# Kernel tuning notes

Hardware: AMD Instinct MI355X
Metric: run time of the kernel (lower is better)

## Reference

```python
import math
import jax, jax.numpy as jnp
import numpy as np

N_NODES = 100000
N_EDGES = 1200000
N_BASIS = 20
HIDDEN = 50
SILU_NORM = 1.679  # e3nn normalize2mom constant for silu
LMAX_SH = 5
MID_LS = (0, 1, 2, 3, 4)          # middle = 1x0e+1x1o+1x2e+1x3o+1x4e (dim 25)
OUT_L = 2                          # out = 1x2e (dim 5)
TP2_PATHS = ((0, 2), (1, 1), (1, 3), (2, 0), (2, 2), (2, 4), (3, 1), (3, 3), (3, 5), (4, 2), (4, 4))
NUM_NEIGHBORS = 6


def _fact(n):
    return math.factorial(n)


def _cg(j1, m1, j2, m2, j3, m3):
    # Racah formula for Clebsch-Gordan coefficients (complex SH, Condon-Shortley).
    if m1 + m2 != m3:
        return 0.0
    pref = math.sqrt((2 * j3 + 1) * _fact(j1 + j2 - j3) * _fact(j1 - j2 + j3) * _fact(-j1 + j2 + j3) / _fact(j1 + j2 + j3 + 1))
    pref *= math.sqrt(_fact(j1 + m1) * _fact(j1 - m1) * _fact(j2 + m2) * _fact(j2 - m2) * _fact(j3 + m3) * _fact(j3 - m3))
    s = 0.0
    for k in range(j1 + j2 - j3 + 1):
        d = (k, j1 + j2 - j3 - k, j1 - m1 - k, j2 + m2 - k, j3 - j2 + m1 + k, j3 - j1 - m2 + k)
        if min(d) < 0:
            continue
        den = 1.0
        for q in d:
            den *= _fact(q)
        s += (-1.0) ** k / den
    return pref * s


def _u_real(l):
    # change of basis complex SH -> real SH, rows indexed by real m=-l..l
    U = np.zeros((2 * l + 1, 2 * l + 1), dtype=np.complex128)
    U[l, l] = 1.0
    rt2 = math.sqrt(2.0)
    for m in range(1, l + 1):
        U[l + m, l + m] = (-1.0) ** m / rt2
        U[l + m, l - m] = 1.0 / rt2
        U[l - m, l + m] = -1j * (-1.0) ** m / rt2
        U[l - m, l - m] = 1j / rt2
    return U


def _w3j_real(j1, j2, j3):
    # real-basis Wigner 3j tensor (real for even j1+j2+j3, which holds for all paths here)
    Wc = np.zeros((2 * j1 + 1, 2 * j2 + 1, 2 * j3 + 1), dtype=np.complex128)
    for m1 in range(-j1, j1 + 1):
        for m2 in range(-j2, j2 + 1):
            m3 = -(m1 + m2)
            if abs(m3) <= j3:
                Wc[j1 + m1, j2 + m2, j3 + m3] = (-1.0) ** (j1 - j2 - m3) / math.sqrt(2 * j3 + 1) * _cg(j1, m1, j2, m2, j3, -m3)
    U1, U2, U3 = _u_real(j1).conj(), _u_real(j2).conj(), _u_real(j3).conj()
    Wr = np.einsum('abc,ia,jb,kc->ijk', Wc, U1, U2, U3)
    return np.ascontiguousarray(Wr.real.astype(np.float32))


W3J_TP1 = {l: _w3j_real(0, l, l) for l in MID_LS}
W3J_TP2 = {p: _w3j_real(p[0], p[1], OUT_L) for p in TP2_PATHS}


def spherical_harmonics(vec):
    # vec [E,3] -> component-normalized real SH for l=0..5, concatenated [E,36]
    r = jnp.sqrt(jnp.sum(vec * vec, axis=1))
    x, y, z = vec[:, 0] / r, vec[:, 1] / r, vec[:, 2] / r
    phi = jnp.arctan2(y, x)
    s = jnp.sqrt(jnp.clip(1.0 - z * z, 0.0, 1.0))
    # associated Legendre P[l][m] without Condon-Shortley phase
    P = [[None] * (l + 1) for l in range(LMAX_SH + 1)]
    P[0][0] = jnp.ones_like(z)
    for m in range(1, LMAX_SH + 1):
        P[m][m] = (2 * m - 1) * s * P[m - 1][m - 1]
    for m in range(0, LMAX_SH):
        P[m + 1][m] = (2 * m + 1) * z * P[m][m]
    for l in range(2, LMAX_SH + 1):
        for m in range(0, l - 1):
            P[l][m] = ((2 * l - 1) * z * P[l - 1][m] - (l - 1 + m) * P[l - 2][m]) / (l - m)
    blocks = []
    for l in range(LMAX_SH + 1):
        comps = []
        for m in range(-l, l + 1):
            am = abs(m)
            c = math.sqrt((2 * l + 1) * _fact(l - am) / _fact(l + am)) * (math.sqrt(2.0) if m != 0 else 1.0)
            if m < 0:
                ang = jnp.sin(am * phi)
            elif m > 0:
                ang = jnp.cos(am * phi)
            else:
                ang = jnp.ones_like(phi)
            comps.append(c * P[l][am] * ang)
        blocks.append(jnp.stack(comps, axis=1))
    return jnp.concatenate(blocks, axis=1)


def soft_one_hot(d):
    # e3nn soft_one_hot_linspace(basis='smooth_finite', cutoff=True), start=0, end=3
    values = jnp.linspace(0.0, 3.0, N_BASIS + 2)
    step = values[1] - values[0]
    values = values[1:-1]
    diff = (d[:, None] - values[None, :]) / step

    def sus(t):
        safe = jnp.where(t > 0, t, 1.0)
        return jnp.where(t > 0, jnp.exp(-1.0 / safe), 0.0)

    return 1.14136 * math.exp(2.0) * sus(diff + 1.0) * sus(1.0 - diff)


def tp1(x_scalar, sh, w):
    # FullyConnectedTensorProduct(1x0e, sh, middle) with external per-edge weights w [E,5]
    outs = []
    for i, l in enumerate(MID_LS):
        W = W3J_TP1[l][0]                       # [2l+1, 2l+1]
        alpha = math.sqrt(2 * l + 1)            # sqrt(dim_out / fan_in), fan_in = 1
        shl = sh[:, l * l:(l + 1) * (l + 1)]
        outs.append(alpha * w[:, i:i + 1] * x_scalar * (shl @ W))
    return jnp.concatenate(outs, axis=1)        # [E, 25]


def tp2(feat, sh, w):
    # FullyConnectedTensorProduct(middle, sh, 1x2e) with internal weights w [11]
    alpha = math.sqrt((2 * OUT_L + 1) / len(TP2_PATHS))
    out = jnp.zeros((feat.shape[0], 2 * OUT_L + 1), dtype=feat.dtype)
    for p, (l1, l2) in enumerate(TP2_PATHS):
        W = W3J_TP2[(l1, l2)]                   # [2l1+1, 2l2+1, 5]
        f = feat[:, l1 * l1:(l1 + 1) * (l1 + 1)]
        s = sh[:, l2 * l2:(l2 + 1) * (l2 + 1)]
        tmp = jnp.einsum('ei,ijk->ejk', f, W)
        out = out + (alpha * w[p]) * jnp.einsum('ejk,ej->ek', tmp, s)
    return out                                   # [E, 5]


def _forward(x, pos, edge_index, mlp_w1, mlp_w2, tp2_w):
    N = pos.shape[0]
    edge_from = edge_index[:, 0]
    edge_to = edge_index[:, 1]
    Co = jnp.argmax(jnp.bincount(edge_to, length=N))          # torch.mode(edge_to)
    edge_vec = pos[edge_to] - pos[edge_from]
    sh = spherical_harmonics(edge_vec)                         # [E, 36]
    dist = jnp.linalg.norm(edge_vec, axis=1)
    emb = soft_one_hot(dist)                                   # [E, 20]
    h = jax.nn.silu(emb @ mlp_w1 / math.sqrt(N_BASIS)) * SILU_NORM
    tp_w = h @ mlp_w2 / math.sqrt(HIDDEN)                      # [E, 5]
    feat = tp1(x[edge_to], sh, tp_w)                           # [E, 25]
    node = jax.ops.segment_sum(feat, edge_from, num_segments=N) / math.sqrt(float(NUM_NEIGHBORS))
    feat2 = tp2(node[edge_to], sh, tp2_w)                      # [E, 5]
    node2 = jax.ops.segment_sum(feat2, edge_from, num_segments=N)
    return node2[Co]                                           # [5]


def setup_inputs():
    N, E = N_NODES, N_EDGES
    key = jax.random.key(0)
    k = jax.random.split(key, 7)
    pos = 1.5 * jax.random.normal(k[0], (N, 3), dtype=jnp.float32)
    x = jax.random.normal(k[1], (N, 1), dtype=jnp.float32)
    ef = jax.random.randint(k[2], (E,), 0, N, dtype=jnp.int32)
    off = jax.random.randint(k[3], (E,), 1, N, dtype=jnp.int32)
    et = (ef + off) % N                                        # no self loops -> nonzero edge_vec
    edge_index = jnp.stack([ef, et], axis=1)
    mlp_w1 = jax.random.normal(k[4], (N_BASIS, HIDDEN), dtype=jnp.float32)
    mlp_w2 = jax.random.normal(k[5], (HIDDEN, len(MID_LS)), dtype=jnp.float32)
    tp2_w = jax.random.normal(k[6], (len(TP2_PATHS),), dtype=jnp.float32)
    return {'x': x, 'pos': pos, 'edge_index': edge_index, 'mlp_w1': mlp_w1, 'mlp_w2': mlp_w2, 'tp2_w': tp2_w}


def reference(x, pos, edge_index, mlp_w1, mlp_w2, tp2_w):
    return _forward(x, pos, edge_index, mlp_w1, mlp_w2, tp2_w)
```

## Files before the change

kernel.cpp:

```cpp
#include <hip/hip_runtime.h>
#include <math.h>

#define CAP   2048
#define NW3J  (2080*8)


struct WSPtrs {
  unsigned* counts;
  int* flag;
  unsigned long long* key;
  int* co_count;
  int* s_count;
  int* co_edges;
  float* node_acc;
  float* w3j1;
  float* w3j2;
  size_t zero_bytes;
};

__host__ __device__ inline WSPtrs make_ws(char* ws, int N, int Nw, int use_xcc){
  WSPtrs p;
  size_t o = 0;
  p.counts   = (unsigned*)(ws + o);
  o += use_xcc ? (size_t)8 * Nw * 4 : (size_t)N * 4;
  p.flag     = (int*)(ws + o); o += (size_t)N * 4;
  o = (o + 7) & ~(size_t)7;
  p.key      = (unsigned long long*)(ws + o); o += 8;
  p.co_count = (int*)(ws + o); o += 4;
  p.s_count  = (int*)(ws + o); o += 4;
  p.co_edges = (int*)(ws + o); o += (size_t)CAP * 4;
  p.node_acc = (float*)(ws + o); o += (size_t)CAP * 25 * 4;
  p.w3j1     = (float*)(ws + o); o += 165 * 4;
  p.w3j2     = (float*)(ws + o); o += 1915 * 4;
  p.zero_bytes = o;
  return p;
}


__device__ double cg_coef_lut(int j1,int m1,int j2,int m2,int j3,int m3, const double* __restrict__ fact){
  if (m1 + m2 != m3) return 0.0;
  double pref = sqrt((2.0*j3+1.0) * fact[j1+j2-j3] * fact[j1-j2+j3] * fact[-j1+j2+j3]
                     / fact[j1+j2+j3+1]);
  pref *= sqrt(fact[j1+m1]*fact[j1-m1]*fact[j2+m2]*fact[j2-m2]*fact[j3+m3]*fact[j3-m3]);
  double s = 0.0;
  for (int k = 0; k <= j1+j2-j3; ++k){
    int d2 = j1-m1-k, d3 = j2+m2-k, d4 = j3-j2+m1+k, d5 = j3-j1-m2+k;
    if (d2 < 0 || d3 < 0 || d4 < 0 || d5 < 0) continue;
    double den = fact[k]*fact[j1+j2-j3-k]*fact[d2]*fact[d3]*fact[d4]*fact[d5];
    s += ((k & 1) ? -1.0 : 1.0) / den;
  }
  return pref * s;
}

__device__ double wigner_c_val_lut(int j1,int j2,int j3,int m1,int m2,int m3, const double* __restrict__ fact){
  if (m1+m2+m3 != 0) return 0.0;
  int e = j1 - j2 - m3;
  double sign = (e & 1) ? -1.0 : 1.0;
  return sign / sqrt(2.0*j3+1.0) * cg_coef_lut(j1,m1,j2,m2,j3,-m3,fact);
}

__device__ int conjU_row(int l, int i, int* cols, double* re, double* im){
  int mr = i - l;
  const double irt2 = 0.70710678118654752440;
  if (mr == 0){ cols[0]=l; re[0]=1.0; im[0]=0.0; return 1; }
  int m = mr > 0 ? mr : -mr;
  double sgn = (m & 1) ? -1.0 : 1.0;
  if (mr > 0){
    cols[0]=l+m; re[0]=sgn*irt2; im[0]=0.0;
    cols[1]=l-m; re[1]=irt2;     im[1]=0.0;
  } else {
    cols[0]=l+m; re[0]=0.0; im[0]= sgn*irt2;
    cols[1]=l-m; re[1]=0.0; im[1]=-irt2;
  }
  return 2;
}

__device__ void wigner_term(int gid, float* __restrict__ w3j1, float* __restrict__ w3j2,
                            const double* __restrict__ sfact){
  int entry = gid >> 3;
  int combo = gid & 7;
  if (entry >= 165 + 1915) return;
  int j1, j2, j3, ii, jj, kk;
  float* dst;
  if (entry < 165){
    const int l1off[5] = {0,1,10,35,84};
    int l = 4;
    for (int q = 1; q < 5; ++q) if (entry < l1off[q]){ l = q-1; break; }
    int t = entry - l1off[l];
    int n = 2*l+1;
    j1 = 0; j2 = l; j3 = l;
    ii = 0; jj = t / n; kk = t % n;
    dst = &w3j1[entry];
  } else {
    int t2 = entry - 165;
    const int pl1[11]  = {0,1,1,2,2,2,3,3,3,4,4};
    const int pl2[11]  = {2,1,3,0,2,4,1,3,5,2,4};
    const int poff[11] = {0,25,70,175,200,325,550,655,900,1285,1510};
    int p = 10;
    for (int q = 1; q < 11; ++q) if (t2 < poff[q]){ p = q-1; break; }
    int t = t2 - poff[p];
    j1 = pl1[p]; j2 = pl2[p]; j3 = 2;
    int n2q = 2*j2+1;
    ii = t / (n2q*5); int rem = t % (n2q*5); jj = rem / 5; kk = rem % 5;
    dst = &w3j2[t2];
  }
  int c1[2], c2[2], c3[2];
  double r1[2], i1[2], r2[2], i2[2], r3[2], i3[2];
  int n1 = conjU_row(j1, ii, c1, r1, i1);
  int n2 = conjU_row(j2, jj, c2, r2, i2);
  int n3 = conjU_row(j3, kk, c3, r3, i3);
  int a = (combo >> 2) & 1, b = (combo >> 1) & 1, c = combo & 1;
  if (a >= n1 || b >= n2 || c >= n3) return;
  int m1 = c1[a]-j1, m2 = c2[b]-j2, m3 = c3[c]-j3;
  if (m1 + m2 + m3 != 0) return;
  double wc = wigner_c_val_lut(j1,j2,j3,m1,m2,m3,sfact);
  if (wc == 0.0) return;
  double pr = r1[a]*r2[b] - i1[a]*i2[b];
  double pi = r1[a]*i2[b] + i1[a]*r2[b];
  double qr = pr*r3[c] - pi*i3[c];
  atomicAdd(dst, (float)(wc*qr));
}


__device__ void compute_sh36f(float ex, float ey, float ez, float* __restrict__ sh){
  float r = sqrtf(ex*ex + ey*ey + ez*ez);
  float x = ex/r, y = ey/r, z = ez/r;
  float t = 1.0f - z*z;
  t = t < 0.0f ? 0.0f : (t > 1.0f ? 1.0f : t);
  float s = sqrtf(t);
  float rxy = sqrtf(x*x + y*y);
  float c1, s1;
  if (rxy > 1e-30f){ c1 = x/rxy; s1 = y/rxy; } else { c1 = 1.0f; s1 = 0.0f; }
  float cm[6], sm[6];
  cm[0] = 1.0f; sm[0] = 0.0f;
  for (int m = 1; m <= 5; ++m){
    cm[m] = cm[m-1]*c1 - sm[m-1]*s1;
    sm[m] = sm[m-1]*c1 + cm[m-1]*s1;
  }
  float P[6][6];
  P[0][0] = 1.0f;
  for (int m=1;m<=5;m++) P[m][m] = (float)(2*m-1)*s*P[m-1][m-1];
  for (int m=0;m<5;m++)  P[m+1][m] = (float)(2*m+1)*z*P[m][m];
  for (int l=2;l<=5;l++)
    for (int m=0;m<=l-2;m++)
      P[l][m] = ((float)(2*l-1)*z*P[l-1][m] - (float)(l-1+m)*P[l-2][m])/(float)(l-m);
  const float rt2 = 1.41421356237309504880f;
  for (int l=0;l<=5;l++){
    for (int m=-l;m<=l;m++){
      int am = m < 0 ? -m : m;
      float ratio = 1.0f;
      for (int k = l-am+1; k <= l+am; ++k) ratio *= (float)k;
      float c = sqrtf((float)(2*l+1)/ratio);
      if (m != 0) c *= rt2;
      float ang = (m < 0) ? sm[am] : ((m > 0) ? cm[am] : 1.0f);
      sh[l*l + m + l] = c * P[l][am] * ang;
    }
  }
}

__device__ void feat_edge(int f, int t, const int* __restrict__ flag,
                          const float* __restrict__ pos, const float* __restrict__ x,
                          const float* __restrict__ w1, const float* __restrict__ w2,
                          const float* w3j1, float* __restrict__ node_acc){
  int slot = flag[f] - 1;
  if (slot < 0 || slot >= CAP) return;

  float ex = pos[3*t+0] - pos[3*f+0];
  float ey = pos[3*t+1] - pos[3*f+1];
  float ez = pos[3*t+2] - pos[3*f+2];
  float sh[36];
  compute_sh36f(ex,ey,ez,sh);
  float d = sqrtf(ex*ex+ey*ey+ez*ez);

  float emb[20];
  const float step = 3.0f/21.0f;
  const float cemb = 1.14136f * 7.38905609893065f;
  for (int jb=0;jb<20;jb++){
    float v = step*(float)(jb+1);
    float diff = (d - v)/step;
    float a = diff + 1.0f, b = 1.0f - diff;
    float sa = (a > 0.0f) ? __expf(-1.0f/a) : 0.0f;
    float sb = (b > 0.0f) ? __expf(-1.0f/b) : 0.0f;
    emb[jb] = cemb * sa * sb;
  }
  float tw[5] = {0,0,0,0,0};
  const float is20 = 0.22360679774997896964f;
  const float is50 = 0.14142135623730950488f;
  for (int kk=0;kk<50;kk++){
    float z = 0.0f;
    for (int jb=0;jb<20;jb++) z += emb[jb]*w1[jb*50+kk];
    z *= is20;
    float hk = (z / (1.0f + __expf(-z))) * 1.679f;
    for (int i=0;i<5;i++) tw[i] += hk * w2[kk*5+i];
  }
  for (int i=0;i<5;i++) tw[i] *= is50;

  float xs = x[t];
  const int w1off[5] = {0,1,10,35,84};
  const float alphal[5] = {1.0f, 1.73205080756887729353f, 2.23606797749978969641f,
                           2.64575131106459059050f, 3.0f};
  int fo = 0;
  for (int l=0;l<5;l++){
    int nl = 2*l+1;
    float scale = alphal[l] * tw[l] * xs;
    for (int kq=0;kq<nl;kq++){
      float acc = 0.0f;
      for (int jq=0;jq<nl;jq++) acc += sh[l*l+jq]*w3j1[w1off[l]+jq*nl+kq];
      atomicAdd(&node_acc[slot*25 + fo + kq], scale*acc);
    }
    fo += nl;
  }
}

__device__ void tp2_task(int e, int p, const int2* __restrict__ ei, const int* __restrict__ flag,
                         const float* __restrict__ pos, const float* __restrict__ node_acc,
                         const float* w3j2, const float* __restrict__ tp2w,
                         float* __restrict__ acc){
  const float inv_sqrt6 = 0.40824829046386301637f;
  const float alpha2    = 0.67419986246324704794f;
  const int pl1[11]  = {0,1,1,2,2,2,3,3,3,4,4};
  const int pl2[11]  = {2,1,3,0,2,4,1,3,5,2,4};
  const int poff[11] = {0,25,70,175,200,325,550,655,900,1285,1510};
  int2 fe = ei[e];
  int f = fe.x, t = fe.y;
  int slot = flag[t] - 1;
  if (slot < 0 || slot >= CAP) return;
  float ex = pos[3*t+0] - pos[3*f+0];
  float ey = pos[3*t+1] - pos[3*f+1];
  float ez = pos[3*t+2] - pos[3*f+2];
  float sh[36];
  compute_sh36f(ex,ey,ez,sh);
  int l1 = pl1[p], l2 = pl2[p], n1 = 2*l1+1, n2 = 2*l2+1;
  const float* W = w3j2 + poff[p];
  float wp = alpha2 * tp2w[p];
  for (int i=0;i<n1;i++){
    float fi = node_acc[slot*25 + l1*l1 + i] * inv_sqrt6;
    for (int j=0;j<n2;j++){
      float fs = wp*fi*sh[l2*l2+j];
      const float* Wij = W + (i*n2+j)*5;
      for (int k=0;k<5;k++) acc[k] += fs*Wij[k];
    }
  }
}


__global__ void count_w3j_kernel(const int2* __restrict__ ei, unsigned* __restrict__ counts,
                                 float* __restrict__ w3j1, float* __restrict__ w3j2,
                                 int N, int Nw, int E, int use_xcc){
  __shared__ double sfact[16];
  if (threadIdx.x == 0){
    double rr = 1.0;
    sfact[0] = 1.0;
    for (int i = 1; i < 16; ++i){ rr *= (double)i; sfact[i] = rr; }
  }
  __syncthreads();
  int tid = blockIdx.x*blockDim.x + threadIdx.x;
  if (tid < NW3J)
    wigner_term(tid, w3j1, w3j2, sfact);
  if (tid >= E) return;
  int v = ei[tid].y;
  if (use_xcc){
    unsigned xcc;
    asm volatile("s_getreg_b32 %0, hwreg(HW_REG_XCC_ID)" : "=s"(xcc));
    unsigned inc = 1u << ((v & 3) * 8);
    __hip_atomic_fetch_add(&counts[(size_t)(xcc & 7) * Nw + (v >> 2)], inc,
                           __ATOMIC_RELAXED, __HIP_MEMORY_SCOPE_WORKGROUP);
  } else {
    atomicAdd(&counts[v], 1u);
  }
}

__global__ void argmax_kernel(const unsigned* __restrict__ counts, unsigned long long* __restrict__ key,
                              int N, int Nw, int use_xcc){
  __shared__ unsigned long long sred[256];
  int i = blockIdx.x*blockDim.x + threadIdx.x;
  unsigned long long best = 0;
  if (use_xcc){
    if (i < Nw){
      unsigned s0=0, s1=0, s2=0, s3=0;
      for (int r = 0; r < 8; ++r){
        unsigned w = counts[(size_t)r*Nw + i];
        s0 += w & 0xffu; s1 += (w>>8) & 0xffu; s2 += (w>>16) & 0xffu; s3 += (w>>24) & 0xffu;
      }
      unsigned cs[4] = {s0, s1, s2, s3};
      for (int q = 0; q < 4; ++q){
        int idx = i*4 + q;
        if (idx < N){
          unsigned long long k = ((unsigned long long)cs[q] << 32) | (unsigned)(N-1-idx);
          if (k > best) best = k;
        }
      }
    }
  } else {
    if (i < N)
      best = ((unsigned long long)counts[i] << 32) | (unsigned)(N-1-i);
  }
  sred[threadIdx.x] = best;
  __syncthreads();
  for (int s = 128; s > 0; s >>= 1){
    if (threadIdx.x < s){
      unsigned long long o = sred[threadIdx.x+s];
      if (o > sred[threadIdx.x]) sred[threadIdx.x] = o;
    }
    __syncthreads();
  }
  if (threadIdx.x == 0) atomicMax(key, sred[0]);
}

__global__ void find_co_kernel(const int2* __restrict__ ei, const unsigned long long* __restrict__ key,
                               int* __restrict__ flag, int* __restrict__ co_count,
                               int* __restrict__ s_count, int* __restrict__ co_edges, int N, int E){
  int e = blockIdx.x*blockDim.x + threadIdx.x;
  if (e >= E) return;
  int Co = N - 1 - (int)(unsigned int)(*key & 0xffffffffull);
  int2 fe = ei[e];
  if (fe.x != Co) return;
  int p = atomicAdd(co_count, 1);
  if (p < CAP) co_edges[p] = e;
  int v = fe.y;
  if (atomicCAS(&flag[v], 0, -1) == 0){
    int slot = atomicAdd(s_count, 1);
    flag[v] = (slot < CAP) ? (slot + 1) : 0;
  }
}

__global__ void collect_feat_kernel(const int2* __restrict__ ei, const int* __restrict__ flag,
                                    const float* __restrict__ pos, const float* __restrict__ x,
                                    const float* __restrict__ w1, const float* __restrict__ w2,
                                    const float* __restrict__ w3j1g, float* __restrict__ node_acc,
                                    int E){
  __shared__ float sw3j1[165];
  for (int i = threadIdx.x; i < 165; i += blockDim.x) sw3j1[i] = w3j1g[i];
  __syncthreads();
  int e = blockIdx.x*blockDim.x + threadIdx.x;
  if (e >= E) return;
  int2 fe = ei[e];
  if (flag[fe.x] > 0)
    feat_edge(fe.x, fe.y, flag, pos, x, w1, w2, sw3j1, node_acc);
}

__global__ void out_kernel(const int2* __restrict__ ei, const int* __restrict__ flag,
                           const float* __restrict__ pos, const float* __restrict__ node_acc,
                           const float* __restrict__ w3j2g, const float* __restrict__ tp2w,
                           const int* __restrict__ co_count, const int* __restrict__ co_edges,
                           float* __restrict__ out){
  __shared__ float sw3j2[1915];
  __shared__ float red[256*5];
  for (int i = threadIdx.x; i < 1915; i += blockDim.x) sw3j2[i] = w3j2g[i];
  __syncthreads();
  float acc[5] = {0,0,0,0,0};
  int n = *co_count; if (n > CAP) n = CAP;
  int tasks = n * 11;
  for (int task = threadIdx.x; task < tasks; task += blockDim.x)
    tp2_task(co_edges[task/11], task%11, ei, flag, pos, node_acc, sw3j2, tp2w, acc);
  for (int k=0;k<5;k++) red[threadIdx.x*5+k] = acc[k];
  __syncthreads();
  if (threadIdx.x < 5){
    float s = 0.0f;
    for (int t2=0;t2<256;t2++) s += red[t2*5+threadIdx.x];
    out[threadIdx.x] = s;
  }
}


extern "C" void kernel_launch(void* const* d_in, const int* in_sizes, int n_in,
                              void* d_out, int out_size, void* d_ws, size_t ws_size,
                              hipStream_t stream){
  const int2*  ei2  = (const int2*)d_in[2];
  const float* xp   = (const float*)d_in[0];
  const float* posp = (const float*)d_in[1];
  const float* w1p  = (const float*)d_in[3];
  const float* w2p  = (const float*)d_in[4];
  const float* tpwp = (const float*)d_in[5];
  float* outp = (float*)d_out;
  char* wsp = (char*)d_ws;
  int N = in_sizes[0];
  int E = in_sizes[2] / 2;
  int Nw = (N + 3) / 4;

  int use_xcc = 1;
  {
    WSPtrs p = make_ws(wsp, N, Nw, 1);
    if (p.zero_bytes + 64 > ws_size) use_xcc = 0;
  }
  WSPtrs P = make_ws(wsp, N, Nw, use_xcc);

  hipMemsetAsync(d_ws, 0, P.zero_bytes, stream);

  int eblocks = (E + 255)/256;
  int nblocks = (N + 255)/256;
  count_w3j_kernel  <<<eblocks, 256, 0, stream>>>(ei2, P.counts, P.w3j1, P.w3j2, N, Nw, E, use_xcc);
  argmax_kernel     <<<nblocks, 256, 0, stream>>>(P.counts, P.key, N, Nw, use_xcc);
  find_co_kernel    <<<eblocks, 256, 0, stream>>>(ei2, P.key, P.flag, P.co_count, P.s_count,
                                                  P.co_edges, N, E);
  collect_feat_kernel<<<eblocks, 256, 0, stream>>>(ei2, P.flag, posp, xp, w1p, w2p, P.w3j1,
                                                   P.node_acc, E);
  out_kernel        <<<1, 256, 0, stream>>>(ei2, P.flag, posp, P.node_acc, P.w3j2, tpwp,
                                            P.co_count, P.co_edges, outp);
}
```

Before: 177.2 us.

## Privatize edge-count histogram in LDS slices and fold workspace zeroing into kernel

Replaces the per-XCC global atomic histogram with block-private LDS histograms. Each block pair covers one edge chunk, and each block counts the half of the nodes that fits in shared memory. The per-chunk slices are written to global memory and summed in the argmax kernel. Zeroing of flags, keys and the accumulator moves into the counting kernel, dropping the separate memset. Wigner coefficients are now computed per entry without atomics. The cost is that every edge is read twice and the argmax pass must reduce up to 128 slices, which means more global memory traffic.

```diff
diff --git a/kernel.cpp b/kernel.cpp
--- a/kernel.cpp
+++ b/kernel.cpp
@@ -1,12 +1,12 @@
 #include <hip/hip_runtime.h>
 #include <math.h>
 
-#define CAP   2048
-#define NW3J  (2080*8)
+#define CAP 2048
+#define HALF_MAX 12544
 
 
 struct WSPtrs {
-  unsigned* counts;
+  unsigned* slices;
   int* flag;
   unsigned long long* key;
   int* co_count;
@@ -15,14 +15,15 @@
   float* node_acc;
   float* w3j1;
   float* w3j2;
-  size_t zero_bytes;
+  size_t fb_zero_bytes;
+  size_t total_bytes;
 };
 
-__host__ __device__ inline WSPtrs make_ws(char* ws, int N, int Nw, int use_xcc){
+__host__ __device__ inline WSPtrs make_ws(char* ws, int N, int half, int C, int fb){
   WSPtrs p;
   size_t o = 0;
-  p.counts   = (unsigned*)(ws + o);
-  o += use_xcc ? (size_t)8 * Nw * 4 : (size_t)N * 4;
+  p.slices   = (unsigned*)(ws + o);
+  o += fb ? (size_t)N * 4 : (size_t)C * 2 * half * 4;
   p.flag     = (int*)(ws + o); o += (size_t)N * 4;
   o = (o + 7) & ~(size_t)7;
   p.key      = (unsigned long long*)(ws + o); o += 8;
@@ -30,9 +31,10 @@
   p.s_count  = (int*)(ws + o); o += 4;
   p.co_edges = (int*)(ws + o); o += (size_t)CAP * 4;
   p.node_acc = (float*)(ws + o); o += (size_t)CAP * 25 * 4;
+  p.fb_zero_bytes = o;
   p.w3j1     = (float*)(ws + o); o += 165 * 4;
   p.w3j2     = (float*)(ws + o); o += 1915 * 4;
-  p.zero_bytes = o;
+  p.total_bytes = o;
   return p;
 }
 
@@ -75,10 +77,8 @@
   return 2;
 }
 
-__device__ void wigner_term(int gid, float* __restrict__ w3j1, float* __restrict__ w3j2,
-                            const double* __restrict__ sfact){
-  int entry = gid >> 3;
-  int combo = gid & 7;
+__device__ void wigner_entry(int entry, const double* __restrict__ sfact,
+                             float* __restrict__ w3j1, float* __restrict__ w3j2){
   if (entry >= 165 + 1915) return;
   int j1, j2, j3, ii, jj, kk;
   float* dst;
@@ -109,16 +109,19 @@
   int n1 = conjU_row(j1, ii, c1, r1, i1);
   int n2 = conjU_row(j2, jj, c2, r2, i2);
   int n3 = conjU_row(j3, kk, c3, r3, i3);
-  int a = (combo >> 2) & 1, b = (combo >> 1) & 1, c = combo & 1;
-  if (a >= n1 || b >= n2 || c >= n3) return;
-  int m1 = c1[a]-j1, m2 = c2[b]-j2, m3 = c3[c]-j3;
-  if (m1 + m2 + m3 != 0) return;
-  double wc = wigner_c_val_lut(j1,j2,j3,m1,m2,m3,sfact);
-  if (wc == 0.0) return;
-  double pr = r1[a]*r2[b] - i1[a]*i2[b];
-  double pi = r1[a]*i2[b] + i1[a]*r2[b];
-  double qr = pr*r3[c] - pi*i3[c];
-  atomicAdd(dst, (float)(wc*qr));
+  double acc = 0.0;
+  for (int combo = 0; combo < 8; ++combo){
+    int a = (combo >> 2) & 1, b = (combo >> 1) & 1, c = combo & 1;
+    if (a >= n1 || b >= n2 || c >= n3) continue;
+    int m1 = c1[a]-j1, m2 = c2[b]-j2, m3 = c3[c]-j3;
+    if (m1 + m2 + m3 != 0) continue;
+    double wc = wigner_c_val_lut(j1,j2,j3,m1,m2,m3,sfact);
+    if (wc == 0.0) continue;
+    double pr = r1[a]*r2[b] - i1[a]*i2[b];
+    double pi = r1[a]*i2[b] + i1[a]*r2[b];
+    acc += wc * (pr*r3[c] - pi*i3[c]);
+  }
+  *dst = (float)acc;
 }
 
 
@@ -244,9 +247,51 @@
 }
 
 
-__global__ void count_w3j_kernel(const int2* __restrict__ ei, unsigned* __restrict__ counts,
-                                 float* __restrict__ w3j1, float* __restrict__ w3j2,
-                                 int N, int Nw, int E, int use_xcc){
+__global__ __launch_bounds__(1024)
+void count_w3j_kernel(const int2* __restrict__ ei, unsigned* __restrict__ slices,
+                      int* __restrict__ flag, unsigned long long* __restrict__ key,
+                      int* __restrict__ co_count, int* __restrict__ s_count,
+                      float* __restrict__ node_acc,
+                      float* __restrict__ w3j1, float* __restrict__ w3j2,
+                      int N, int half, int E, int C){
+  __shared__ double sfact[16];
+  __shared__ unsigned hist[HALF_MAX];
+  if (threadIdx.x == 0){
+    double rr = 1.0;
+    sfact[0] = 1.0;
+    for (int i = 1; i < 16; ++i){ rr *= (double)i; sfact[i] = rr; }
+  }
+  for (int i = threadIdx.x; i < half; i += blockDim.x) hist[i] = 0;
+  __syncthreads();
+
+  int gtid = blockIdx.x*blockDim.x + threadIdx.x;
+  int gsize = gridDim.x*blockDim.x;
+
+  if (gtid < 2080) wigner_entry(gtid, sfact, w3j1, w3j2);
+
+  for (int i = gtid; i < N; i += gsize) flag[i] = 0;
+  for (int i = gtid; i < CAP*25; i += gsize) node_acc[i] = 0.0f;
+  if (gtid == 0){ *key = 0ull; *co_count = 0; *s_count = 0; }
+
+  int c = blockIdx.x >> 1;
+  int r = blockIdx.x & 1;
+  int wbase = r * half;
+  size_t e0 = (size_t)c * (size_t)E / (size_t)C;
+  size_t e1 = (size_t)(c+1) * (size_t)E / (size_t)C;
+  for (size_t e = e0 + threadIdx.x; e < e1; e += blockDim.x){
+    int v = ei[e].y;
+    int lw = (v >> 2) - wbase;
+    if (lw >= 0 && lw < half)
+      atomicAdd(&hist[lw], 1u << ((v & 3) * 8));
+  }
+  __syncthreads();
+
+  unsigned* dst = slices + (size_t)(c*2 + r) * half;
+  for (int i = threadIdx.x; i < half; i += blockDim.x) dst[i] = hist[i];
+}
+
+__global__ void count_fb_kernel(const int2* __restrict__ ei, unsigned* __restrict__ counts,
+                                float* __restrict__ w3j1, float* __restrict__ w3j2, int E){
   __shared__ double sfact[16];
   if (threadIdx.x == 0){
     double rr = 1.0;
@@ -255,45 +300,32 @@
   }
   __syncthreads();
   int tid = blockIdx.x*blockDim.x + threadIdx.x;
-  if (tid < NW3J)
-    wigner_term(tid, w3j1, w3j2, sfact);
-  if (tid >= E) return;
-  int v = ei[tid].y;
-  if (use_xcc){
-    unsigned xcc;
-    asm volatile("s_getreg_b32 %0, hwreg(HW_REG_XCC_ID)" : "=s"(xcc));
-    unsigned inc = 1u << ((v & 3) * 8);
-    __hip_atomic_fetch_add(&counts[(size_t)(xcc & 7) * Nw + (v >> 2)], inc,
-                           __ATOMIC_RELAXED, __HIP_MEMORY_SCOPE_WORKGROUP);
-  } else {
-    atomicAdd(&counts[v], 1u);
-  }
-}
-
-__global__ void argmax_kernel(const unsigned* __restrict__ counts, unsigned long long* __restrict__ key,
-                              int N, int Nw, int use_xcc){
+  if (tid < 2080) wigner_entry(tid, sfact, w3j1, w3j2);
+  if (tid < E) atomicAdd(&counts[ei[tid].y], 1u);
+}
+
+__global__ void argmax_kernel(const unsigned* __restrict__ slices, unsigned long long* __restrict__ key,
+                              int N, int Nw, int half, int C, int fb){
   __shared__ unsigned long long sred[256];
-  int i = blockIdx.x*blockDim.x + threadIdx.x;
+  int w = blockIdx.x*blockDim.x + threadIdx.x;
   unsigned long long best = 0;
-  if (use_xcc){
-    if (i < Nw){
-      unsigned s0=0, s1=0, s2=0, s3=0;
-      for (int r = 0; r < 8; ++r){
-        unsigned w = counts[(size_t)r*Nw + i];
-        s0 += w & 0xffu; s1 += (w>>8) & 0xffu; s2 += (w>>16) & 0xffu; s3 += (w>>24) & 0xffu;
+  if (fb){
+    if (w < N)
+      best = ((unsigned long long)slices[w] << 32) | (unsigned)(N-1-w);
+  } else if (w < Nw){
+    int r = (w >= half) ? 1 : 0;
+    int lw = w - r*half;
+    unsigned sum = 0;
+    for (int c = 0; c < C; ++c)
+      sum += slices[(size_t)(c*2 + r) * half + lw];
+    for (int q = 0; q < 4; ++q){
+      int idx = w*4 + q;
+      if (idx < N){
+        unsigned cnt = (sum >> (q*8)) & 0xffu;
+        unsigned long long k = ((unsigned long long)cnt << 32) | (unsigned)(N-1-idx);
+        if (k > best) best = k;
       }
-      unsigned cs[4] = {s0, s1, s2, s3};
-      for (int q = 0; q < 4; ++q){
-        int idx = i*4 + q;
-        if (idx < N){
-          unsigned long long k = ((unsigned long long)cs[q] << 32) | (unsigned)(N-1-idx);
-          if (k > best) best = k;
-        }
-      }
-    }
-  } else {
-    if (i < N)
-      best = ((unsigned long long)counts[i] << 32) | (unsigned)(N-1-i);
+    }
   }
   sred[threadIdx.x] = best;
   __syncthreads();
@@ -376,21 +408,31 @@
   char* wsp = (char*)d_ws;
   int N = in_sizes[0];
   int E = in_sizes[2] / 2;
-  int Nw = (N + 3) / 4;
-
-  int use_xcc = 1;
-  {
-    WSPtrs p = make_ws(wsp, N, Nw, 1);
-    if (p.zero_bytes + 64 > ws_size) use_xcc = 0;
-  }
-  WSPtrs P = make_ws(wsp, N, Nw, use_xcc);
-
-  hipMemsetAsync(d_ws, 0, P.zero_bytes, stream);
+  int Nw = (N + 3) >> 2;
+  int half = (Nw + 1) >> 1;
+
+  int fb = (half > HALF_MAX) ? 1 : 0;
+  int C = 0;
+  if (!fb){
+    for (int cand = 128; cand >= 8; cand >>= 1){
+      WSPtrs p = make_ws(wsp, N, half, cand, 0);
+      if (p.total_bytes + 64 <= ws_size){ C = cand; break; }
+    }
+    if (C == 0) fb = 1;
+  }
+  WSPtrs P = make_ws(wsp, N, half, fb ? 1 : C, fb);
 
   int eblocks = (E + 255)/256;
-  int nblocks = (N + 255)/256;
-  count_w3j_kernel  <<<eblocks, 256, 0, stream>>>(ei2, P.counts, P.w3j1, P.w3j2, N, Nw, E, use_xcc);
-  argmax_kernel     <<<nblocks, 256, 0, stream>>>(P.counts, P.key, N, Nw, use_xcc);
+  if (fb){
+    hipMemsetAsync(d_ws, 0, P.fb_zero_bytes, stream);
+    count_fb_kernel<<<eblocks, 256, 0, stream>>>(ei2, P.slices, P.w3j1, P.w3j2, E);
+  } else {
+    count_w3j_kernel<<<2*C, 1024, 0, stream>>>(ei2, P.slices, P.flag, P.key,
+                                               P.co_count, P.s_count, P.node_acc,
+                                               P.w3j1, P.w3j2, N, half, E, C);
+  }
+  int ablocks = fb ? (N + 255)/256 : (Nw + 255)/256;
+  argmax_kernel     <<<ablocks, 256, 0, stream>>>(P.slices, P.key, N, Nw, half, C, fb);
   find_co_kernel    <<<eblocks, 256, 0, stream>>>(ei2, P.key, P.flag, P.co_count, P.s_count,
                                                   P.co_edges, N, E);
   collect_feat_kernel<<<eblocks, 256, 0, stream>>>(ei2, P.flag, posp, xp, w1p, w2p, P.w3j1,
```

After: 166.5 us. -6.0%, faster.
